# Optimization experiments

Measured on AMD Instinct MI355X. Metric: run time of the kernel, lower is better.

Reference implementation:

```python
import jax, jax.numpy as jnp
import numpy as np
import itertools

# LeViT-style Attention config (matches init_kwargs)
DIM = 256
KD = 32          # key_dim
H = 8            # num_heads
AR = 4           # attn_ratio
RES = 14
N = RES * RES    # 196 tokens
D = AR * KD      # per-head value dim = 128
DH = D * H       # 1024
NHKD = KD * H    # 256
HID = DH + 2 * NHKD  # 1536 = qkv width
EPS = 1e-5
SCALE = KD ** -0.5
BATCH = 256


def _bias_idxs():
    # Same construction as the torch module: index into table of unique abs offsets.
    points = list(itertools.product(range(RES), range(RES)))
    offs = {}
    idxs = []
    for p1 in points:
        for p2 in points:
            o = (abs(p1[0] - p2[0]), abs(p1[1] - p2[1]))
            if o not in offs:
                offs[o] = len(offs)
            idxs.append(offs[o])
    return np.asarray(idxs, dtype=np.int32).reshape(N, N), len(offs)


def _bn(x, g, b):
    # BatchNorm1d in training mode over the flattened (B*N, F) batch dim.
    mu = x.mean(axis=0)
    var = jnp.var(x, axis=0)  # biased, as torch BN uses for normalization
    return (x - mu) * jax.lax.rsqrt(var + EPS) * g + b


def setup_inputs() -> dict:
    key = jax.random.key(0)
    ks = jax.random.split(key, 8)
    idxs_np, n_off = _bias_idxs()  # n_off == 196 for RES=14
    x = jax.random.normal(ks[0], (BATCH, N, DIM), dtype=jnp.float32)
    Wqkv = jax.random.normal(ks[1], (HID, DIM), dtype=jnp.float32) * 0.02
    g1 = 1.0 + 0.1 * jax.random.normal(ks[2], (HID,), dtype=jnp.float32)
    b1 = 0.1 * jax.random.normal(ks[3], (HID,), dtype=jnp.float32)
    # init is zeros in the module; use small randn so the bias path is exercised
    bias_table = 0.1 * jax.random.normal(ks[4], (H, n_off), dtype=jnp.float32)
    Wproj = jax.random.normal(ks[5], (DIM, DH), dtype=jnp.float32) * 0.02
    # bn_weight_init=0 in module; use nonzero so output/grads are nontrivial
    g2 = 1.0 + 0.1 * jax.random.normal(ks[6], (DIM,), dtype=jnp.float32)
    b2 = 0.1 * jax.random.normal(ks[7], (DIM,), dtype=jnp.float32)
    return {
        "x": x, "Wqkv": Wqkv, "g1": g1, "b1": b1,
        "bias_table": bias_table, "Wproj": Wproj, "g2": g2, "b2": b2,
        "idxs": jnp.asarray(idxs_np),
    }


def reference(x, Wqkv, g1, b1, bias_table, Wproj, g2, b2, idxs):
    B, Ntok, C = x.shape
    # qkv = Linear_BN(x): bias-free linear then BN over flattened (B*N, HID)
    h = jnp.einsum('bnc,hc->bnh', x, Wqkv)
    h = _bn(h.reshape(B * Ntok, HID), g1, b1).reshape(B, Ntok, H, -1)
    q = h[..., :KD].transpose(0, 2, 1, 3)            # (B,H,N,KD)
    k = h[..., KD:2 * KD].transpose(0, 2, 1, 3)      # (B,H,N,KD)
    v = h[..., 2 * KD:].transpose(0, 2, 1, 3)        # (B,H,N,D)
    bias = bias_table[:, idxs]                       # (H,N,N) relative-position bias gather
    attn = jnp.einsum('bhnd,bhmd->bhnm', q, k) * SCALE + bias
    attn = jax.nn.softmax(attn, axis=-1)
    o = jnp.einsum('bhnm,bhmd->bhnd', attn, v)
    o = o.transpose(0, 2, 1, 3).reshape(B, Ntok, DH)
    # proj = Hardswish -> Linear_BN(dh, dim)
    o = o * jnp.clip(o + 3.0, 0.0, 6.0) / 6.0
    o = jnp.einsum('bnd,cd->bnc', o, Wproj)
    o = _bn(o.reshape(B * Ntok, C), g2, b2).reshape(B, Ntok, C)
    return o
```

## Files before the change

kernel.cpp:

```cpp
#include <hip/hip_runtime.h>

typedef _Float16 f16;
typedef __attribute__((ext_vector_type(8))) _Float16 half8;
typedef __attribute__((ext_vector_type(4))) _Float16 half4;
typedef __attribute__((ext_vector_type(4))) float   f4;

#define NTOK   196
#define MROWS  50176
#define HIDN   1536
#define HPC    192
#define DHD    1024
#define EPSV   1e-5f
#define SCALEV 0.17677669529663687f

#define GLD16(gp, lp) __builtin_amdgcn_global_load_lds( \
    (const __attribute__((address_space(1))) unsigned int*)(gp), \
    (__attribute__((address_space(3))) unsigned int*)(lp), 16, 0, 0)

__device__ inline int swz8(int row) { return (((row & 7) ^ ((row >> 3) & 7))) * 8; }

__global__ void cvt_f32_f16(const float* __restrict__ src, f16* __restrict__ dst, int n4)
{
    int i = blockIdx.x * blockDim.x + threadIdx.x;
    if (i < n4) {
        float4 v = *(const float4*)&src[i * 4];
        half4 h = { (f16)v.x, (f16)v.y, (f16)v.z, (f16)v.w };
        *(half4*)&dst[i * 4] = h;
    }
}

__global__ void build_bias(const float* __restrict__ bt, const int* __restrict__ idxs,
                           f16* __restrict__ bf)
{
    int i = blockIdx.x * 256 + threadIdx.x;
    if (i >= 8 * 208 * 224) return;
    int k = i % 224, q = (i / 224) % 208, h = i / (224 * 208);
    float v = -30000.f;
    if (q < NTOK && k < NTOK) v = bt[h * NTOK + idxs[q * NTOK + k]];
    bf[i] = (f16)v;
}

__global__ __launch_bounds__(256) void gemm1_qkv(
    const f16* __restrict__ A, const f16* __restrict__ B,
    f16* __restrict__ C, float* __restrict__ gsum, float* __restrict__ gsq)
{
    const int K = 256, ldc = HIDN;
    __shared__ f16 As[128 * 32];
    __shared__ f16 Bs[128 * 32];
    __shared__ float ssum[128], ssq[128];

    const int t = threadIdx.x;
    const int m0 = blockIdx.x * 128, n0 = blockIdx.y * 128;
    const int wid = t >> 6, lane = t & 63, quad = lane >> 4, lm = lane & 15;
    const int wm = (wid >> 1) * 64, wn = (wid & 1) * 64;

    const int lr = lane >> 2, lc = (lane & 3) * 8;
    f16* As0 = &As[(wid * 2 + 0) * 512];
    f16* As1 = &As[(wid * 2 + 1) * 512];
    f16* Bs0 = &Bs[(wid * 2 + 0) * 512];
    f16* Bs1 = &Bs[(wid * 2 + 1) * 512];
    const f16* Ab = A + (long)(m0 + wid * 32 + lr) * K + lc;
    const f16* Bb = B + (long)(n0 + wid * 32 + lr) * K + lc;

    f4 acc[4][4] = {};

    for (int k0 = 0; k0 < K; k0 += 32) {
        GLD16(Ab + k0,          As0);
        GLD16(Ab + 16 * K + k0, As1);
        GLD16(Bb + k0,          Bs0);
        GLD16(Bb + 16 * K + k0, Bs1);
        __syncthreads();
        half8 a[4], b[4];
        #pragma unroll
        for (int i = 0; i < 4; ++i) a[i] = *(const half8*)&As[(wm + i*16 + lm) * 32 + quad * 8];
        #pragma unroll
        for (int j = 0; j < 4; ++j) b[j] = *(const half8*)&Bs[(wn + j*16 + lm) * 32 + quad * 8];
        #pragma unroll
        for (int i = 0; i < 4; ++i)
            #pragma unroll
            for (int j = 0; j < 4; ++j)
                acc[i][j] = __builtin_amdgcn_mfma_f32_16x16x32_f16(a[i], b[j], acc[i][j], 0, 0, 0);
        __syncthreads();
    }

    if (t < 128) { ssum[t] = 0.f; ssq[t] = 0.f; }
    __syncthreads();

    #pragma unroll
    for (int j = 0; j < 4; ++j) {
        int nl = wn + j*16 + lm;
        float psum = 0.f, psq = 0.f;
        #pragma unroll
        for (int i = 0; i < 4; ++i) {
            #pragma unroll
            for (int r = 0; r < 4; ++r) {
                int ml = wm + i*16 + quad*4 + r;
                float v = acc[i][j][r];
                f16 uh = (f16)v;
                float vb = (float)uh;
                C[(long)(m0 + ml) * ldc + n0 + nl] = uh;
                psum += vb; psq += vb * vb;
            }
        }
        atomicAdd(&ssum[nl], psum);
        atomicAdd(&ssq[nl], psq);
    }
    __syncthreads();
    if (t < 128) {
        atomicAdd(&gsum[n0 + t], ssum[t]);
        atomicAdd(&gsq[n0 + t],  ssq[t]);
    }
}

__global__ __launch_bounds__(256) void gemm2_proj(
    const f16* __restrict__ A, const f16* __restrict__ B,
    float* __restrict__ C, float* __restrict__ gsum, float* __restrict__ gsq)
{
    const int K = 1024, ldc = 256;
    __shared__ f16 As[128 * 32];
    __shared__ f16 Bs[128 * 32];
    __shared__ float ssum[128], ssq[128];

    const int t = threadIdx.x;
    const int m0 = blockIdx.x * 128, n0 = blockIdx.y * 128;
    const int wid = t >> 6, lane = t & 63, quad = lane >> 4, lm = lane & 15;
    const int wm = (wid >> 1) * 64, wn = (wid & 1) * 64;

    const int lr = lane >> 2, lc = (lane & 3) * 8;
    f16* As0 = &As[(wid * 2 + 0) * 512];
    f16* As1 = &As[(wid * 2 + 1) * 512];
    f16* Bs0 = &Bs[(wid * 2 + 0) * 512];
    f16* Bs1 = &Bs[(wid * 2 + 1) * 512];
    const f16* Ab = A + (long)(m0 + wid * 32 + lr) * K + lc;
    const f16* Bb = B + (long)(n0 + wid * 32 + lr) * K + lc;

    f4 acc[4][4] = {};

    for (int k0 = 0; k0 < K; k0 += 32) {
        GLD16(Ab + k0,          As0);
        GLD16(Ab + 16 * K + k0, As1);
        GLD16(Bb + k0,          Bs0);
        GLD16(Bb + 16 * K + k0, Bs1);
        __syncthreads();
        half8 a[4], b[4];
        #pragma unroll
        for (int i = 0; i < 4; ++i) a[i] = *(const half8*)&As[(wm + i*16 + lm) * 32 + quad * 8];
        #pragma unroll
        for (int j = 0; j < 4; ++j) b[j] = *(const half8*)&Bs[(wn + j*16 + lm) * 32 + quad * 8];
        #pragma unroll
        for (int i = 0; i < 4; ++i)
            #pragma unroll
            for (int j = 0; j < 4; ++j)
                acc[i][j] = __builtin_amdgcn_mfma_f32_16x16x32_f16(a[i], b[j], acc[i][j], 0, 0, 0);
        __syncthreads();
    }

    if (t < 128) { ssum[t] = 0.f; ssq[t] = 0.f; }
    __syncthreads();

    #pragma unroll
    for (int j = 0; j < 4; ++j) {
        int nl = wn + j*16 + lm;
        float psum = 0.f, psq = 0.f;
        #pragma unroll
        for (int i = 0; i < 4; ++i) {
            #pragma unroll
            for (int r = 0; r < 4; ++r) {
                int ml = wm + i*16 + quad*4 + r;
                float v = acc[i][j][r];
                C[(long)(m0 + ml) * ldc + n0 + nl] = v;
                psum += v; psq += v * v;
            }
        }
        atomicAdd(&ssum[nl], psum);
        atomicAdd(&ssq[nl], psq);
    }
    __syncthreads();
    if (t < 128) {
        atomicAdd(&gsum[n0 + t], ssum[t]);
        atomicAdd(&gsq[n0 + t],  ssq[t]);
    }
}

__global__ void bn_fin(const float* __restrict__ gsum, const float* __restrict__ gsq,
                       const float* __restrict__ g, const float* __restrict__ b,
                       float* __restrict__ a_out, float* __restrict__ s_out, int nch)
{
    int c = blockIdx.x * blockDim.x + threadIdx.x;
    if (c >= nch) return;
    float inv  = 1.f / (float)MROWS;
    float mean = gsum[c] * inv;
    float var  = gsq[c] * inv - mean * mean;
    float a    = g[c] * rsqrtf(var + EPSV);
    a_out[c] = a;
    s_out[c] = b[c] - mean * a;
}

__global__ __launch_bounds__(512) void attn_kernel(
    const f16* __restrict__ hbuf, const float* __restrict__ a1, const float* __restrict__ s1,
    const f16* __restrict__ bf, f16* __restrict__ obuf)
{
    __shared__ f16   qs[208][32];
    __shared__ f16   ks[208][32];
    __shared__ f16   vT[128][256];
    __shared__ f16   ps[8][16][256];
    __shared__ float af[192], sf[192];

    const int t  = threadIdx.x;
    const int bb = blockIdx.x >> 3;
    const int hh = blockIdx.x & 7;
    const int wid = t >> 6, lane = t & 63, quad = lane >> 4, lm = lane & 15;

    if (t < 192) { af[t] = a1[hh * HPC + t]; sf[t] = s1[hh * HPC + t]; }
    half8 z8 = {};
    for (int i = t; i < 4096; i += 512) *(half8*)&vT[i >> 5][(i & 31) * 8] = z8;
    for (int i = t; i < 4096; i += 512) *(half8*)&ps[i >> 9][(i >> 5) & 15][(i & 31) * 8] = z8;
    for (int i = t; i < 12 * 32; i += 512) { qs[196 + (i >> 5)][i & 31] = (f16)0.f;
                                             ks[196 + (i >> 5)][i & 31] = (f16)0.f; }
    __syncthreads();

    {
        int t8 = t & 7;
        for (int rr = t >> 3; rr < NTOK; rr += 64) {
            const f16* hrow = hbuf + (long)(bb * NTOK + rr) * HIDN + hh * HPC;
            int sr = swz8(rr);
            #pragma unroll
            for (int cc = 0; cc < 3; ++cc) {
                int cb = (t8 + cc * 8) * 8;
                half8 raw = *(const half8*)(hrow + cb);
                f16 ov[8];
                #pragma unroll
                for (int e = 0; e < 8; ++e)
                    ov[e] = (f16)((float)raw[e] * af[cb + e] + sf[cb + e]);
                if (cb < 32) {
                    #pragma unroll
                    for (int e = 0; e < 8; ++e) qs[rr][(cb + e + sr) & 31] = ov[e];
                } else if (cb < 64) {
                    #pragma unroll
                    for (int e = 0; e < 8; ++e) ks[rr][(cb - 32 + e + sr) & 31] = ov[e];
                } else {
                    #pragma unroll
                    for (int e = 0; e < 8; ++e) {
                        int c = cb - 64 + e;
                        vT[c][(rr + swz8(c)) & 255] = ov[e];
                    }
                }
            }
        }
    }
    __syncthreads();

    const int nmt = (wid + 8 < 13) ? 2 : 1;
    half8 ap[2][7];
    const f16* bfh = bf + hh * 208 * 224;

    for (int pass = 0; pass < nmt; ++pass) {
        const int mt = wid + pass * 8;
        int qrowA = mt * 16 + lm;
        half8 aq = *(const half8*)&qs[qrowA][(quad * 8 + swz8(qrowA)) & 31];
        f4 sreg[13];
        #pragma unroll
        for (int nt = 0; nt < 13; ++nt) {
            int krow = nt * 16 + lm;
            half8 bk = *(const half8*)&ks[krow][(quad * 8 + swz8(krow)) & 31];
            f4 z = {};
            sreg[nt] = __builtin_amdgcn_mfma_f32_16x16x32_f16(aq, bk, z, 0, 0, 0);
        }
        #pragma unroll
        for (int nt = 0; nt < 13; ++nt) {
            int kc = nt * 16 + lm;
            #pragma unroll
            for (int r = 0; r < 4; ++r) {
                int qrow = mt * 16 + quad * 4 + r;
                float bias_v = (float)bfh[qrow * 224 + kc];
                sreg[nt][r] = sreg[nt][r] * SCALEV + bias_v;
            }
        }
        float rinv[4];
        #pragma unroll
        for (int r = 0; r < 4; ++r) {
            float m = sreg[0][r];
            #pragma unroll
            for (int nt = 1; nt < 13; ++nt) m = fmaxf(m, sreg[nt][r]);
            #pragma unroll
            for (int d = 1; d < 16; d <<= 1) m = fmaxf(m, __shfl_xor(m, d));
            float s = 0.f;
            #pragma unroll
            for (int nt = 0; nt < 13; ++nt) {
                float e = __expf(sreg[nt][r] - m);
                sreg[nt][r] = e;
                s += e;
            }
            #pragma unroll
            for (int d = 1; d < 16; d <<= 1) s += __shfl_xor(s, d);
            rinv[r] = 1.f / s;
        }
        #pragma unroll
        for (int nt = 0; nt < 13; ++nt)
            #pragma unroll
            for (int r = 0; r < 4; ++r) {
                int q = quad * 4 + r;
                ps[wid][q][(nt * 16 + lm + swz8(q)) & 255] = (f16)(sreg[nt][r] * rinv[r]);
            }
        #pragma unroll
        for (int k7 = 0; k7 < 7; ++k7)
            ap[pass][k7] = *(const half8*)&ps[wid][lm][(k7 * 32 + quad * 8 + swz8(lm)) & 255];
    }

    #pragma unroll
    for (int ct = 0; ct < 8; ++ct) {
        int c = ct * 16 + lm;
        int sc = swz8(c);
        f4 oa0 = {}, oa1 = {};
        #pragma unroll
        for (int k7 = 0; k7 < 7; ++k7) {
            half8 bv = *(const half8*)&vT[c][(k7 * 32 + quad * 8 + sc) & 255];
            oa0 = __builtin_amdgcn_mfma_f32_16x16x32_f16(ap[0][k7], bv, oa0, 0, 0, 0);
            if (nmt == 2)
                oa1 = __builtin_amdgcn_mfma_f32_16x16x32_f16(ap[1][k7], bv, oa1, 0, 0, 0);
        }
        #pragma unroll
        for (int r = 0; r < 4; ++r) {
            int qrow = wid * 16 + quad * 4 + r;
            if (qrow < 196) {
                float v  = oa0[r];
                float hs = v * fminf(fmaxf(v + 3.f, 0.f), 6.f) * (1.f / 6.f);
                obuf[(long)(bb * NTOK + qrow) * DHD + hh * 128 + c] = (f16)hs;
            }
        }
        if (nmt == 2) {
            #pragma unroll
            for (int r = 0; r < 4; ++r) {
                int qrow = (wid + 8) * 16 + quad * 4 + r;
                if (qrow < 196) {
                    float v  = oa1[r];
                    float hs = v * fminf(fmaxf(v + 3.f, 0.f), 6.f) * (1.f / 6.f);
                    obuf[(long)(bb * NTOK + qrow) * DHD + hh * 128 + c] = (f16)hs;
                }
            }
        }
    }
}

__global__ __launch_bounds__(256) void bn_apply(
    float* __restrict__ out, const float* __restrict__ a2, const float* __restrict__ s2)
{
    __shared__ float aL[256], sL[256];
    int t = threadIdx.x;
    aL[t] = a2[t]; sL[t] = s2[t];
    __syncthreads();
    long total = (long)MROWS * 256 / 4;
    for (long i = (long)blockIdx.x * 256 + t; i < total; i += (long)gridDim.x * 256) {
        float4 v = *(float4*)&out[i * 4];
        int cb = (int)((i * 4) & 255);
        v.x = v.x * aL[cb + 0] + sL[cb + 0];
        v.y = v.y * aL[cb + 1] + sL[cb + 1];
        v.z = v.z * aL[cb + 2] + sL[cb + 2];
        v.w = v.w * aL[cb + 3] + sL[cb + 3];
        *(float4*)&out[i * 4] = v;
    }
}

extern "C" void kernel_launch(void* const* d_in, const int* in_sizes, int n_in,
                              void* d_out, int out_size, void* d_ws, size_t ws_size,
                              hipStream_t stream)
{
    (void)in_sizes; (void)n_in; (void)out_size; (void)ws_size;
    const float* x          = (const float*)d_in[0];
    const float* Wqkv       = (const float*)d_in[1];
    const float* g1         = (const float*)d_in[2];
    const float* b1         = (const float*)d_in[3];
    const float* bias_table = (const float*)d_in[4];
    const float* Wproj      = (const float*)d_in[5];
    const float* g2         = (const float*)d_in[6];
    const float* b2         = (const float*)d_in[7];
    const int*   idxs       = (const int*)d_in[8];
    float*       out        = (float*)d_out;

    char* ws = (char*)d_ws;
    f16* hbuf = (f16*)ws;
    f16* obuf = (f16*)(ws + 154140672LL);
    f16* xh   = (f16*)(ws + 154140672LL);
    f16* wqh  = (f16*)(ws + 154140672LL + 25690112LL);
    f16* wph  = (f16*)ws;
    float* stats = (float*)(ws + 256901120LL);
    float* gsum1 = stats;            float* gsq1 = stats + 1536;
    float* gsum2 = stats + 3072;     float* gsq2 = stats + 3328;
    float* a1 = stats + 3584;        float* s1 = a1 + 1536;
    float* a2 = s1 + 1536;           float* s2 = a2 + 256;
    f16* bias_full = (f16*)(ws + 256901120LL + 65536LL);

    hipMemsetAsync(stats, 0, 3584 * sizeof(float), stream);

    cvt_f32_f16<<<12544, 256, 0, stream>>>(x, xh, 3211264);
    cvt_f32_f16<<<384,   256, 0, stream>>>(Wqkv, wqh, 98304);
    build_bias<<<1456, 256, 0, stream>>>(bias_table, idxs, bias_full);

    gemm1_qkv<<<dim3(392, 12), 256, 0, stream>>>(xh, wqh, hbuf, gsum1, gsq1);
    bn_fin<<<6, 256, 0, stream>>>(gsum1, gsq1, g1, b1, a1, s1, 1536);

    attn_kernel<<<2048, 512, 0, stream>>>(hbuf, a1, s1, bias_full, obuf);

    cvt_f32_f16<<<256, 256, 0, stream>>>(Wproj, wph, 65536);

    gemm2_proj<<<dim3(392, 2), 256, 0, stream>>>(obuf, wph, out, gsum2, gsq2);
    bn_fin<<<1, 256, 0, stream>>>(gsum2, gsq2, g2, b2, a2, s2, 256);

    bn_apply<<<1024, 256, 0, stream>>>(out, a2, s2);
}
```

Measured before the change: 479.1 us.

## Keep softmax probabilities in registers via transposed S and drop LDS staging

```diff
diff --git a/kernel.cpp b/kernel.cpp
--- a/kernel.cpp
+++ b/kernel.cpp
@@ -196,14 +196,12 @@
     s_out[c] = b[c] - mean * a;
 }
 
-__global__ __launch_bounds__(512) void attn_kernel(
+__global__ __launch_bounds__(512, 4) void attn_kernel(
     const f16* __restrict__ hbuf, const float* __restrict__ a1, const float* __restrict__ s1,
     const f16* __restrict__ bf, f16* __restrict__ obuf)
 {
-    __shared__ f16   qs[208][32];
     __shared__ f16   ks[208][32];
     __shared__ f16   vT[128][256];
-    __shared__ f16   ps[8][16][256];
     __shared__ float af[192], sf[192];
 
     const int t  = threadIdx.x;
@@ -214,9 +212,7 @@
     if (t < 192) { af[t] = a1[hh * HPC + t]; sf[t] = s1[hh * HPC + t]; }
     half8 z8 = {};
     for (int i = t; i < 4096; i += 512) *(half8*)&vT[i >> 5][(i & 31) * 8] = z8;
-    for (int i = t; i < 4096; i += 512) *(half8*)&ps[i >> 9][(i >> 5) & 15][(i & 31) * 8] = z8;
-    for (int i = t; i < 12 * 32; i += 512) { qs[196 + (i >> 5)][i & 31] = (f16)0.f;
-                                             ks[196 + (i >> 5)][i & 31] = (f16)0.f; }
+    for (int i = t; i < 12 * 32; i += 512) ks[196 + (i >> 5)][i & 31] = (f16)0.f;
     __syncthreads();
 
     {
@@ -226,16 +222,14 @@
             int sr = swz8(rr);
             #pragma unroll
             for (int cc = 0; cc < 3; ++cc) {
-                int cb = (t8 + cc * 8) * 8;
+                int cb = 32 + (t8 + cc * 8) * 8;
+                if (cb >= 192) continue;
                 half8 raw = *(const half8*)(hrow + cb);
                 f16 ov[8];
                 #pragma unroll
                 for (int e = 0; e < 8; ++e)
                     ov[e] = (f16)((float)raw[e] * af[cb + e] + sf[cb + e]);
-                if (cb < 32) {
-                    #pragma unroll
-                    for (int e = 0; e < 8; ++e) qs[rr][(cb + e + sr) & 31] = ov[e];
-                } else if (cb < 64) {
+                if (cb < 64) {
                     #pragma unroll
                     for (int e = 0; e < 8; ++e) ks[rr][(cb - 32 + e + sr) & 31] = ov[e];
                 } else {
@@ -251,91 +245,79 @@
     __syncthreads();
 
     const int nmt = (wid + 8 < 13) ? 2 : 1;
-    half8 ap[2][7];
     const f16* bfh = bf + hh * 208 * 224;
 
     for (int pass = 0; pass < nmt; ++pass) {
         const int mt = wid + pass * 8;
-        int qrowA = mt * 16 + lm;
-        half8 aq = *(const half8*)&qs[qrowA][(quad * 8 + swz8(qrowA)) & 31];
+        const int qrow = mt * 16 + lm;
+
+        long grow = (long)bb * NTOK + qrow;
+        if (grow > (long)(MROWS - 1)) grow = MROWS - 1;
+        half8 qraw = *(const half8*)(hbuf + grow * HIDN + hh * HPC + quad * 8);
+        half8 qf;
+        #pragma unroll
+        for (int e = 0; e < 8; ++e)
+            qf[e] = (f16)((float)qraw[e] * af[quad * 8 + e] + sf[quad * 8 + e]);
+
         f4 sreg[13];
         #pragma unroll
         for (int nt = 0; nt < 13; ++nt) {
             int krow = nt * 16 + lm;
-            half8 bk = *(const half8*)&ks[krow][(quad * 8 + swz8(krow)) & 31];
+            half8 ak = *(const half8*)&ks[krow][(quad * 8 + swz8(krow)) & 31];
             f4 z = {};
-            sreg[nt] = __builtin_amdgcn_mfma_f32_16x16x32_f16(aq, bk, z, 0, 0, 0);
-        }
+            sreg[nt] = __builtin_amdgcn_mfma_f32_16x16x32_f16(ak, qf, z, 0, 0, 0);
+        }
+
+        const f16* brow = bfh + qrow * 224 + quad * 4;
+        float m = -3.0e38f;
         #pragma unroll
         for (int nt = 0; nt < 13; ++nt) {
-            int kc = nt * 16 + lm;
+            half4 b4 = *(const half4*)(brow + nt * 16);
             #pragma unroll
             for (int r = 0; r < 4; ++r) {
-                int qrow = mt * 16 + quad * 4 + r;
-                float bias_v = (float)bfh[qrow * 224 + kc];
-                sreg[nt][r] = sreg[nt][r] * SCALEV + bias_v;
-            }
-        }
-        float rinv[4];
-        #pragma unroll
-        for (int r = 0; r < 4; ++r) {
-            float m = sreg[0][r];
-            #pragma unroll
-            for (int nt = 1; nt < 13; ++nt) m = fmaxf(m, sreg[nt][r]);
-            #pragma unroll
-            for (int d = 1; d < 16; d <<= 1) m = fmaxf(m, __shfl_xor(m, d));
-            float s = 0.f;
+                sreg[nt][r] = sreg[nt][r] * SCALEV + (float)b4[r];
+                m = fmaxf(m, sreg[nt][r]);
+            }
+        }
+        m = fmaxf(m, __shfl_xor(m, 16));
+        m = fmaxf(m, __shfl_xor(m, 32));
+
+        float s = 0.f;
+        half4 ap[13];
+        #pragma unroll
+        for (int nt = 0; nt < 13; ++nt) {
+            float e0 = __expf(sreg[nt][0] - m);
+            float e1 = __expf(sreg[nt][1] - m);
+            float e2 = __expf(sreg[nt][2] - m);
+            float e3 = __expf(sreg[nt][3] - m);
+            s += (e0 + e1) + (e2 + e3);
+            ap[nt] = half4{ (f16)e0, (f16)e1, (f16)e2, (f16)e3 };
+        }
+        s += __shfl_xor(s, 16);
+        s += __shfl_xor(s, 32);
+        float rinv = 1.f / s;
+
+        float rv[4];
+        #pragma unroll
+        for (int r = 0; r < 4; ++r) rv[r] = __shfl(rinv, quad * 4 + r);
+
+        #pragma unroll
+        for (int ct = 0; ct < 8; ++ct) {
+            int c = ct * 16 + lm;
+            int sc = swz8(c);
+            f4 oa = {};
             #pragma unroll
             for (int nt = 0; nt < 13; ++nt) {
-                float e = __expf(sreg[nt][r] - m);
-                sreg[nt][r] = e;
-                s += e;
-            }
-            #pragma unroll
-            for (int d = 1; d < 16; d <<= 1) s += __shfl_xor(s, d);
-            rinv[r] = 1.f / s;
-        }
-        #pragma unroll
-        for (int nt = 0; nt < 13; ++nt)
+                half4 bv = *(const half4*)&vT[c][(nt * 16 + quad * 4 + sc) & 255];
+                oa = __builtin_amdgcn_mfma_f32_16x16x16f16(ap[nt], bv, oa, 0, 0, 0);
+            }
             #pragma unroll
             for (int r = 0; r < 4; ++r) {
-                int q = quad * 4 + r;
-                ps[wid][q][(nt * 16 + lm + swz8(q)) & 255] = (f16)(sreg[nt][r] * rinv[r]);
-            }
-        #pragma unroll
-        for (int k7 = 0; k7 < 7; ++k7)
-            ap[pass][k7] = *(const half8*)&ps[wid][lm][(k7 * 32 + quad * 8 + swz8(lm)) & 255];
-    }
-
-    #pragma unroll
-    for (int ct = 0; ct < 8; ++ct) {
-        int c = ct * 16 + lm;
-        int sc = swz8(c);
-        f4 oa0 = {}, oa1 = {};
-        #pragma unroll
-        for (int k7 = 0; k7 < 7; ++k7) {
-            half8 bv = *(const half8*)&vT[c][(k7 * 32 + quad * 8 + sc) & 255];
-            oa0 = __builtin_amdgcn_mfma_f32_16x16x32_f16(ap[0][k7], bv, oa0, 0, 0, 0);
-            if (nmt == 2)
-                oa1 = __builtin_amdgcn_mfma_f32_16x16x32_f16(ap[1][k7], bv, oa1, 0, 0, 0);
-        }
-        #pragma unroll
-        for (int r = 0; r < 4; ++r) {
-            int qrow = wid * 16 + quad * 4 + r;
-            if (qrow < 196) {
-                float v  = oa0[r];
-                float hs = v * fminf(fmaxf(v + 3.f, 0.f), 6.f) * (1.f / 6.f);
-                obuf[(long)(bb * NTOK + qrow) * DHD + hh * 128 + c] = (f16)hs;
-            }
-        }
-        if (nmt == 2) {
-            #pragma unroll
-            for (int r = 0; r < 4; ++r) {
-                int qrow = (wid + 8) * 16 + quad * 4 + r;
-                if (qrow < 196) {
-                    float v  = oa1[r];
+                int qr = mt * 16 + quad * 4 + r;
+                if (qr < 196) {
+                    float v  = oa[r] * rv[r];
                     float hs = v * fminf(fmaxf(v + 3.f, 0.f), 6.f) * (1.f / 6.f);
-                    obuf[(long)(bb * NTOK + qrow) * DHD + hh * 128 + c] = (f16)hs;
+                    obuf[(long)(bb * NTOK + qr) * DHD + hh * 128 + c] = (f16)hs;
                 }
             }
         }
```

New measurement: 1.028 ms. 2.14x slower.
